# Performance work log

Measured on AMD Instinct MI355X. Metric: run time of the kernel, lower is better.

## Reference

```python
import jax, jax.numpy as jnp
from jax import lax
import numpy as np

IN_CH = 32
OUT_CH = IN_CH // 4  # 8
K = 3

def _branch(x6, axis, w, b, a):
    # x6: [B, C, U, V, H, W]. Fold `axis` into batch, run one batched conv3d
    # over the remaining three spatio-angular dims (kernel 3, pad 1 == SAME),
    # then PReLU and unfold. Mathematically identical to the per-slice loop.
    x = jnp.moveaxis(x6, axis, 1)              # [B, L, C, d1, d2, d3]
    B, L = x.shape[0], x.shape[1]
    xr = x.reshape((B * L,) + x.shape[2:])      # [B*L, C, d1, d2, d3]
    y = lax.conv_general_dilated(
        xr, w, window_strides=(1, 1, 1), padding='SAME',
        dimension_numbers=('NCDHW', 'OIDHW', 'NCDHW'))
    y = y + b[None, :, None, None, None]
    y = jnp.where(y >= 0, y, a * y)             # PReLU (single shared slope)
    y = y.reshape((B, L) + y.shape[1:])         # [B, L, O, d1, d2, d3]
    return jnp.moveaxis(y, 1, axis)             # [B, O, U, V, H, W]

def setup_inputs() -> dict:
    key = jax.random.key(0)
    ks = jax.random.split(key, 9)
    fan_in = IN_CH * K * K * K
    bound = 1.0 / np.sqrt(fan_in)
    x = jax.random.normal(ks[0], (8, IN_CH, 5, 5, 64, 64), dtype=jnp.float32)
    def mk_w(k):
        return jax.random.uniform(k, (OUT_CH, IN_CH, K, K, K), jnp.float32, -bound, bound)
    def mk_b(k):
        return jax.random.uniform(k, (OUT_CH,), jnp.float32, -bound, bound)
    inp = {'x': x}
    for i, name in enumerate(['uvx', 'uvy', 'uxy', 'vxy']):
        inp[f'w_{name}'] = mk_w(ks[1 + 2 * i])
        inp[f'b_{name}'] = mk_b(ks[2 + 2 * i])
        inp[f'a_{name}'] = jnp.full((1,), 0.25, dtype=jnp.float32)  # PReLU init
    return inp

def reference(x, w_uvx, b_uvx, a_uvx, w_uvy, b_uvy, a_uvy,
              w_uxy, b_uxy, a_uxy, w_vxy, b_vxy, a_vxy):
    # x: [B, C, U, V, H, W]
    uvx = _branch(x, 5, w_uvx, b_uvx, a_uvx)  # conv over (U, V, H), slice W
    uvy = _branch(x, 4, w_uvy, b_uvy, a_uvy)  # conv over (U, V, W), slice H
    uxy = _branch(x, 3, w_uxy, b_uxy, a_uxy)  # conv over (U, H, W), slice V
    vxy = _branch(x, 2, w_vxy, b_vxy, a_vxy)  # conv over (V, H, W), slice U
    return jnp.concatenate([uvx, uvy, uxy, vxy], axis=1)
```

## Files before the change

kernel.cpp:

```cpp
#include <hip/hip_runtime.h>

#define B_  8
#define C_  32
#define U_  5
#define V_  5
#define H_  64
#define W_  64

#define SV_ 4096
#define SU_ 20480
#define SC_ 102400
#define SB_ 3276800

#define XROW 4224
#define BT_OFF 54067200ull

typedef short bf16x8 __attribute__((ext_vector_type(8)));
typedef float f32x4 __attribute__((ext_vector_type(4)));

__device__ __forceinline__ unsigned short f2bf(float f) {
    unsigned int u = __builtin_bit_cast(unsigned int, f);
    u = (u + 0x7FFFu + ((u >> 16) & 1u)) >> 16;
    return (unsigned short)u;
}

__device__ __forceinline__ f32x4 mfma16(bf16x8 a, bf16x8 b, f32x4 c) {
    return __builtin_amdgcn_mfma_f32_16x16x32_bf16(a, b, c, 0, 0, 0);
}

__global__ __launch_bounds__(256)
void k_prep(const float* __restrict__ x, unsigned short* __restrict__ xT,
            const float* __restrict__ w0, const float* __restrict__ w1,
            const float* __restrict__ w2, const float* __restrict__ w3,
            unsigned short* __restrict__ btab)
{
    if (blockIdx.x >= 3200) {
        const int f = blockIdx.x - 3200;
        const int br = f / 27;
        const int tap = f % 27;
        const float* wp = (br == 0) ? w0 : (br == 1) ? w1 : (br == 2) ? w2 : w3;
        const int q  = threadIdx.x >> 6;
        const int oc = (threadIdx.x >> 3) & 7;
        const int j  = threadIdx.x & 7;
        btab[(size_t)f * 256 + q * 64 + oc * 8 + j] =
            f2bf(wp[(size_t)oc * 864 + (q * 8 + j) * 27 + tap]);
        return;
    }

    __shared__ float tl[C_ * 4 * 64];
    const int tid = threadIdx.x;
    int blk = blockIdx.x;
    const int hq = blk & 15; blk >>= 4;
    const int v = blk % 5; blk /= 5;
    const int u = blk % 5;
    const int b = blk / 5;
    const int h0 = hq * 4;

    const float* src = x + (size_t)b * SB_ + (size_t)u * SU_ + (size_t)v * SV_ + h0 * 64;
#pragma unroll
    for (int i = 0; i < 8; ++i) {
        const int e = tid + i * 256;
        const int c = e >> 6;
        const int rem = e & 63;
        const int h = rem >> 4;
        const int w4 = (rem & 15) * 4;
        const float4 val = *(const float4*)(src + (size_t)c * SC_ + h * 64 + w4);
        *(float4*)(tl + c * 256 + h * 64 + w4) = val;
    }
    __syncthreads();

    const int h = tid >> 6;
    const int w = tid & 63;
    unsigned short* dst = xT + (size_t)((b * 25 + u * 5 + v) * 64 + h0 + h) * (XROW / 2);
    const uint4 z = make_uint4(0u, 0u, 0u, 0u);
#pragma unroll
    for (int cq = 0; cq < 4; ++cq) {
        unsigned short s[8];
#pragma unroll
        for (int j = 0; j < 8; ++j)
            s[j] = f2bf(tl[(cq * 8 + j) * 256 + h * 64 + w]);
        uint4 o;
        o.x = (unsigned)s[0] | ((unsigned)s[1] << 16);
        o.y = (unsigned)s[2] | ((unsigned)s[3] << 16);
        o.z = (unsigned)s[4] | ((unsigned)s[5] << 16);
        o.w = (unsigned)s[6] | ((unsigned)s[7] << 16);
        *(uint4*)(dst + cq * 528 + (w + 1) * 8) = o;
        if (w == 0)  *(uint4*)(dst + cq * 528 + 0)       = z;
        if (w == 63) *(uint4*)(dst + cq * 528 + 65 * 8)  = z;
    }
}

__global__ __launch_bounds__(512, 2)
void k_main(const unsigned short* __restrict__ xT,
            const unsigned short* __restrict__ btabu,
            const float* __restrict__ bb0, const float* __restrict__ aa0,
            const float* __restrict__ bb1, const float* __restrict__ aa1,
            const float* __restrict__ bb2, const float* __restrict__ aa2,
            const float* __restrict__ bb3, const float* __restrict__ aa3,
            float* __restrict__ out)
{
    __shared__ alignas(16) char wlds[55296];

    const int tid = threadIdx.x;
    const int blk = blockIdx.x;
    const int b   = blk & 7;
    const int i   = blk >> 3;
    const int buv = i >> 3;
    const int hs  = i & 7;
    const int v = buv % 5;
    const int u = buv / 5;
    const int h0 = hs * 8;

    {
        const uint4* g = (const uint4*)btabu;
        uint4* l = (uint4*)wlds;
#pragma unroll
        for (int it = 0; it < 7; ++it) {
            const int e = tid + it * 512;
            if (e < 3456) l[e] = g[e];
        }
    }
    __syncthreads();

    const int wave = tid >> 6;
    const int lane = tid & 63;
    const int n = lane & 15;
    const int q = lane >> 4;
    const int w0 = (wave & 3) * 16;
    const int rbase = (wave >> 2) * 4;
    const int hb = h0 + rbase;

    f32x4 acc[4][4];
#pragma unroll
    for (int a = 0; a < 4; ++a)
#pragma unroll
        for (int j = 0; j < 4; ++j) acc[a][j] = (f32x4)0.f;

    const char* xTb = (const char*)xT;
    const int lane_off = q * 1056 + (w0 + n) * 16;

    auto WF = [&](int f) -> bf16x8 {
        return *(const bf16x8*)(wlds + f * 512 + q * 128 + (n & 7) * 16);
    };
    const bf16x8 zf = {0, 0, 0, 0, 0, 0, 0, 0};

#pragma unroll
    for (int du = 0; du < 3; ++du) {
        const int up = u + du - 1;
        if (up < 0 || up >= 5) continue;
#pragma unroll
        for (int dv = 0; dv < 3; ++dv) {
            const int vp = v + dv - 1;
            if (vp < 0 || vp >= 5) continue;

            const char* base = xTb + (size_t)((b * 25 + up * 5 + vp) * 64) * XROW + lane_off;

#pragma unroll
            for (int dw = 0; dw < 3; ++dw) {
                bf16x8 F[6];
#pragma unroll
                for (int r = 0; r < 6; ++r) {
                    const int hr = hb + r - 1;
                    F[r] = (hr < 0 || hr >= 64) ? zf
                         : *(const bf16x8*)(base + (size_t)hr * XROW + dw * 16);
                }

                if (dw == 1) {
#pragma unroll
                    for (int t = 0; t < 3; ++t) {
                        const bf16x8 Wf = WF(du * 9 + dv * 3 + t);
#pragma unroll
                        for (int hh = 0; hh < 4; ++hh)
                            acc[0][hh] = mfma16(Wf, F[t + hh], acc[0][hh]);
                    }
                }
                {
                    const bf16x8 Wf = WF(27 + du * 9 + dv * 3 + dw);
#pragma unroll
                    for (int hh = 0; hh < 4; ++hh)
                        acc[1][hh] = mfma16(Wf, F[hh + 1], acc[1][hh]);
                }
                if (dv == 1) {
#pragma unroll
                    for (int dh = 0; dh < 3; ++dh) {
                        const bf16x8 Wf = WF(54 + du * 9 + dh * 3 + dw);
#pragma unroll
                        for (int hh = 0; hh < 4; ++hh)
                            acc[2][hh] = mfma16(Wf, F[dh + hh], acc[2][hh]);
                    }
                }
                if (du == 1) {
#pragma unroll
                    for (int dh = 0; dh < 3; ++dh) {
                        const bf16x8 Wf = WF(81 + dv * 9 + dh * 3 + dw);
#pragma unroll
                        for (int hh = 0; hh < 4; ++hh)
                            acc[3][hh] = mfma16(Wf, F[dh + hh], acc[3][hh]);
                    }
                }
            }
        }
    }

    const float alph[4] = { aa0[0], aa1[0], aa2[0], aa3[0] };
    float* op = out + (size_t)b * SB_ + (size_t)u * SU_ + (size_t)v * SV_ + w0 + n;
    const bool act = (q < 2);
#pragma unroll
    for (int br = 0; br < 4; ++br) {
        const float* bp = (br == 0) ? bb0 : (br == 1) ? bb1 : (br == 2) ? bb2 : bb3;
        const f32x4 bv = *(const f32x4*)(bp + (q & 1) * 4);
#pragma unroll
        for (int hh = 0; hh < 4; ++hh) {
            const int h = hb + hh;
#pragma unroll
            for (int r = 0; r < 4; ++r) {
                float val = acc[br][hh][r] + bv[r];
                val = (val >= 0.f) ? val : alph[br] * val;
                if (act)
                    op[(size_t)(br * 8 + q * 4 + r) * SC_ + (size_t)h * 64] = val;
            }
        }
    }
}

extern "C" void kernel_launch(void* const* d_in, const int* in_sizes, int n_in,
                              void* d_out, int out_size, void* d_ws, size_t ws_size,
                              hipStream_t stream) {
    const float* x  = (const float*)d_in[0];
    const float* w0 = (const float*)d_in[1];
    const float* b0 = (const float*)d_in[2];
    const float* a0 = (const float*)d_in[3];
    const float* w1 = (const float*)d_in[4];
    const float* b1 = (const float*)d_in[5];
    const float* a1 = (const float*)d_in[6];
    const float* w2 = (const float*)d_in[7];
    const float* b2 = (const float*)d_in[8];
    const float* a2 = (const float*)d_in[9];
    const float* w3 = (const float*)d_in[10];
    const float* b3 = (const float*)d_in[11];
    const float* a3 = (const float*)d_in[12];
    float* out = (float*)d_out;

    unsigned short* xT = (unsigned short*)d_ws;
    unsigned short* bt = (unsigned short*)((char*)d_ws + BT_OFF);

    k_prep<<<3200 + 108, 256, 0, stream>>>(x, xT, w0, w1, w2, w3, bt);
    k_main<<<1600, 512, 0, stream>>>(
        xT, bt, b0, a0, b1, a1, b2, a2, b3, a3, out);
}
```

Before: 284.7 us.

## Pack branch pairs into shared 16-row MFMA tiles to stop wasting half of each output

Before, each MFMA used 16 output rows but only 8 output channels existed per branch, so half the lanes computed duplicate results that were then discarded. Now branches 0/1 and 2/3 are packed into the 16 rows of shared accumulators. Where the two branches share a tap, a full 16-row weight tile is used. Elsewhere a half-zero tile is used so each branch's extra taps contribute only to its own rows. This roughly halves the number of accumulators, and all lanes now store output. The weight table layout and prep kernel are rebuilt to match, and row loads are trimmed when fewer rows are needed.

Result: faster. 275.2 us (-3.3%).

```diff
diff --git a/kernel.cpp b/kernel.cpp
--- a/kernel.cpp
+++ b/kernel.cpp
@@ -14,6 +14,7 @@
 
 #define XROW 4224
 #define BT_OFF 54067200ull
+#define BT_BYTES 56448
 
 typedef short bf16x8 __attribute__((ext_vector_type(8)));
 typedef float f32x4 __attribute__((ext_vector_type(4)));
@@ -36,14 +37,49 @@
 {
     if (blockIdx.x >= 3200) {
         const int f = blockIdx.x - 3200;
-        const int br = f / 27;
-        const int tap = f % 27;
-        const float* wp = (br == 0) ? w0 : (br == 1) ? w1 : (br == 2) ? w2 : w3;
-        const int q  = threadIdx.x >> 6;
-        const int oc = (threadIdx.x >> 3) & 7;
-        const int j  = threadIdx.x & 7;
-        btab[(size_t)f * 256 + q * 64 + oc * 8 + j] =
-            f2bf(wp[(size_t)oc * 864 + (q * 8 + j) * 27 + tap]);
+        const int tid = threadIdx.x;
+        if (f < 18) {
+            for (int e = tid; e < 512; e += 256) {
+                const int q = e >> 7, row = (e >> 3) & 15, j = e & 7;
+                const int c = q * 8 + j;
+                float val;
+                if (f < 9) {
+                    const int tap = (f / 3) * 9 + (f % 3) * 3 + 1;
+                    val = (row < 8) ? w0[row * 864 + c * 27 + tap]
+                                    : w1[(row - 8) * 864 + c * 27 + tap];
+                } else {
+                    const int tap = 9 + (f - 9);
+                    val = (row < 8) ? w2[row * 864 + c * 27 + tap]
+                                    : w3[(row - 8) * 864 + c * 27 + tap];
+                }
+                btab[f * 512 + e] = f2bf(val);
+            }
+        } else {
+            const bool hi = (f >= 54);
+            const int g = hi ? (f - 54) : (f - 18);
+            const size_t base = (hi ? 37440u : 18432u) / 2 + (size_t)g * 264;
+            for (int e = tid; e < 264; e += 256) {
+                unsigned short outv = 0;
+                if (e < 256) {
+                    const int q = e >> 6, oc = (e >> 3) & 7, j = e & 7;
+                    const int c = q * 8 + j;
+                    float val;
+                    if (g < 18) {
+                        const int p = g >> 1, which = g & 1;
+                        const int tap = (p / 3) * 9 + (p % 3) * 3 + which * 2;
+                        val = hi ? w1[oc * 864 + c * 27 + tap]
+                                 : w0[oc * 864 + c * 27 + tap];
+                    } else {
+                        const int h2 = g - 18;
+                        const int tap = (h2 / 9) * 18 + (h2 % 9);
+                        val = hi ? w3[oc * 864 + c * 27 + tap]
+                                 : w2[oc * 864 + c * 27 + tap];
+                    }
+                    outv = f2bf(val);
+                }
+                btab[base + e] = outv;
+            }
+        }
         return;
     }
 
@@ -99,7 +135,7 @@
             const float* __restrict__ bb3, const float* __restrict__ aa3,
             float* __restrict__ out)
 {
-    __shared__ alignas(16) char wlds[55296];
+    __shared__ alignas(16) char wlds[BT_BYTES];
 
     const int tid = threadIdx.x;
     const int blk = blockIdx.x;
@@ -117,7 +153,7 @@
 #pragma unroll
         for (int it = 0; it < 7; ++it) {
             const int e = tid + it * 512;
-            if (e < 3456) l[e] = g[e];
+            if (e < 3528) l[e] = g[e];
         }
     }
     __syncthreads();
@@ -127,20 +163,28 @@
     const int n = lane & 15;
     const int q = lane >> 4;
     const int w0 = (wave & 3) * 16;
-    const int rbase = (wave >> 2) * 4;
-    const int hb = h0 + rbase;
-
-    f32x4 acc[4][4];
-#pragma unroll
-    for (int a = 0; a < 4; ++a)
-#pragma unroll
-        for (int j = 0; j < 4; ++j) acc[a][j] = (f32x4)0.f;
+    const int hb = h0 + (wave >> 2) * 4;
+    const int hbu = __builtin_amdgcn_readfirstlane(hb);
+
+    f32x4 acc01[4], acc23[4];
+#pragma unroll
+    for (int j = 0; j < 4; ++j) { acc01[j] = (f32x4)0.f; acc23[j] = (f32x4)0.f; }
 
     const char* xTb = (const char*)xT;
     const int lane_off = q * 1056 + (w0 + n) * 16;
 
-    auto WF = [&](int f) -> bf16x8 {
-        return *(const bf16x8*)(wlds + f * 512 + q * 128 + (n & 7) * 16);
+    const int off_full = q * 256 + n * 16;
+    const int off_lo   = (n < 8) ? (q * 128 + n * 16) : 512;
+    const int off_hi   = (n < 8) ? 512 : (q * 128 + (n & 7) * 16);
+
+    auto RF = [&](int f) -> bf16x8 {
+        return *(const bf16x8*)(wlds + f * 1024 + off_full);
+    };
+    auto RL = [&](int g) -> bf16x8 {
+        return *(const bf16x8*)(wlds + 18432 + g * 528 + off_lo);
+    };
+    auto RH = [&](int g) -> bf16x8 {
+        return *(const bf16x8*)(wlds + 37440 + g * 528 + off_hi);
     };
     const bf16x8 zf = {0, 0, 0, 0, 0, 0, 0, 0};
 
@@ -153,72 +197,90 @@
             const int vp = v + dv - 1;
             if (vp < 0 || vp >= 5) continue;
 
-            const char* base = xTb + (size_t)((b * 25 + up * 5 + vp) * 64) * XROW + lane_off;
-
-#pragma unroll
-            for (int dw = 0; dw < 3; ++dw) {
+            const char* rb = xTb + (size_t)((b * 25 + up * 5 + vp) * 64) * XROW;
+            const int p01 = du * 3 + dv;
+            const bool t23 = (du == 1) || (dv == 1);
+
+#pragma unroll
+            for (int bb = 0; bb < 3; ++bb) {
+                const int rlo = (t23 || bb == 1) ? 0 : 1;
+                const int rhi = (t23 || bb == 1) ? 5 : 4;
                 bf16x8 F[6];
 #pragma unroll
                 for (int r = 0; r < 6; ++r) {
-                    const int hr = hb + r - 1;
+                    if (r < rlo || r > rhi) continue;
+                    const int hr = hbu + r - 1;
                     F[r] = (hr < 0 || hr >= 64) ? zf
-                         : *(const bf16x8*)(base + (size_t)hr * XROW + dw * 16);
-                }
-
-                if (dw == 1) {
-#pragma unroll
-                    for (int t = 0; t < 3; ++t) {
-                        const bf16x8 Wf = WF(du * 9 + dv * 3 + t);
+                         : *(const bf16x8*)(rb + (size_t)hr * XROW + lane_off + bb * 16);
+                }
+
+                if (bb == 1) {
+                    const bf16x8 Wl0 = RL(p01 * 2 + 0);
+                    const bf16x8 Wc  = RF(p01);
+                    const bf16x8 Wl2 = RL(p01 * 2 + 1);
+#pragma unroll
+                    for (int hh = 0; hh < 4; ++hh) {
+                        acc01[hh] = mfma16(Wl0, F[0 + hh], acc01[hh]);
+                        acc01[hh] = mfma16(Wc,  F[1 + hh], acc01[hh]);
+                        acc01[hh] = mfma16(Wl2, F[2 + hh], acc01[hh]);
+                    }
+                } else {
+                    const bf16x8 Wh = RH(p01 * 2 + (bb == 2 ? 1 : 0));
+#pragma unroll
+                    for (int hh = 0; hh < 4; ++hh)
+                        acc01[hh] = mfma16(Wh, F[1 + hh], acc01[hh]);
+                }
+
+                if (du == 1 && dv == 1) {
+#pragma unroll
+                    for (int a = 0; a < 3; ++a) {
+                        const bf16x8 Wf = RF(9 + a * 3 + bb);
 #pragma unroll
                         for (int hh = 0; hh < 4; ++hh)
-                            acc[0][hh] = mfma16(Wf, F[t + hh], acc[0][hh]);
-                    }
-                }
-                {
-                    const bf16x8 Wf = WF(27 + du * 9 + dv * 3 + dw);
-#pragma unroll
-                    for (int hh = 0; hh < 4; ++hh)
-                        acc[1][hh] = mfma16(Wf, F[hh + 1], acc[1][hh]);
-                }
-                if (dv == 1) {
-#pragma unroll
-                    for (int dh = 0; dh < 3; ++dh) {
-                        const bf16x8 Wf = WF(54 + du * 9 + dh * 3 + dw);
+                            acc23[hh] = mfma16(Wf, F[a + hh], acc23[hh]);
+                    }
+                } else if (dv == 1) {
+#pragma unroll
+                    for (int a = 0; a < 3; ++a) {
+                        const bf16x8 Wl = RL(18 + (du == 2 ? 9 : 0) + a * 3 + bb);
 #pragma unroll
                         for (int hh = 0; hh < 4; ++hh)
-                            acc[2][hh] = mfma16(Wf, F[dh + hh], acc[2][hh]);
-                    }
-                }
-                if (du == 1) {
-#pragma unroll
-                    for (int dh = 0; dh < 3; ++dh) {
-                        const bf16x8 Wf = WF(81 + dv * 9 + dh * 3 + dw);
+                            acc23[hh] = mfma16(Wl, F[a + hh], acc23[hh]);
+                    }
+                } else if (du == 1) {
+#pragma unroll
+                    for (int a = 0; a < 3; ++a) {
+                        const bf16x8 Wh = RH(18 + (dv == 2 ? 9 : 0) + a * 3 + bb);
 #pragma unroll
                         for (int hh = 0; hh < 4; ++hh)
-                            acc[3][hh] = mfma16(Wf, F[dh + hh], acc[3][hh]);
+                            acc23[hh] = mfma16(Wh, F[a + hh], acc23[hh]);
                     }
                 }
             }
         }
     }
 
-    const float alph[4] = { aa0[0], aa1[0], aa2[0], aa3[0] };
+    const int qh = q >> 1;
+    const int ql = q & 1;
+    const float* bp0 = qh ? bb1 : bb0;
+    const float* bp1 = qh ? bb3 : bb2;
+    const float al0 = qh ? aa1[0] : aa0[0];
+    const float al1 = qh ? aa3[0] : aa2[0];
+    const f32x4 bv0 = *(const f32x4*)(bp0 + ql * 4);
+    const f32x4 bv1 = *(const f32x4*)(bp1 + ql * 4);
+
     float* op = out + (size_t)b * SB_ + (size_t)u * SU_ + (size_t)v * SV_ + w0 + n;
-    const bool act = (q < 2);
-#pragma unroll
-    for (int br = 0; br < 4; ++br) {
-        const float* bp = (br == 0) ? bb0 : (br == 1) ? bb1 : (br == 2) ? bb2 : bb3;
-        const f32x4 bv = *(const f32x4*)(bp + (q & 1) * 4);
-#pragma unroll
-        for (int hh = 0; hh < 4; ++hh) {
-            const int h = hb + hh;
-#pragma unroll
-            for (int r = 0; r < 4; ++r) {
-                float val = acc[br][hh][r] + bv[r];
-                val = (val >= 0.f) ? val : alph[br] * val;
-                if (act)
-                    op[(size_t)(br * 8 + q * 4 + r) * SC_ + (size_t)h * 64] = val;
-            }
+#pragma unroll
+    for (int hh = 0; hh < 4; ++hh) {
+        const int h = hbu + hh;
+#pragma unroll
+        for (int r = 0; r < 4; ++r) {
+            float v0 = acc01[hh][r] + bv0[r];
+            v0 = (v0 >= 0.f) ? v0 : al0 * v0;
+            op[(size_t)(q * 4 + r) * SC_ + (size_t)h * 64] = v0;
+            float v1 = acc23[hh][r] + bv1[r];
+            v1 = (v1 >= 0.f) ? v1 : al1 * v1;
+            op[(size_t)(16 + q * 4 + r) * SC_ + (size_t)h * 64] = v1;
         }
     }
 }
@@ -244,7 +306,7 @@
     unsigned short* xT = (unsigned short*)d_ws;
     unsigned short* bt = (unsigned short*)((char*)d_ws + BT_OFF);
 
-    k_prep<<<3200 + 108, 256, 0, stream>>>(x, xT, w0, w1, w2, w3, bt);
+    k_prep<<<3200 + 90, 256, 0, stream>>>(x, xT, w0, w1, w2, w3, bt);
     k_main<<<1600, 512, 0, stream>>>(
         xT, bt, b0, a0, b1, a1, b2, a2, b3, a3, out);
 }
```
